# Optimization experiments

Measured on AMD Instinct MI355X. Metric: run time of the kernel, lower is better.

The kernel has to match this reference:

```python
import jax, jax.numpy as jnp
import numpy as np

HEADS = 8
SR = 4
EPS = 1e-5


def _ln(x, g, b):
    m = jnp.mean(x, -1, keepdims=True)
    v = jnp.mean(jnp.square(x - m), -1, keepdims=True)
    return (x - m) / jnp.sqrt(v + EPS) * g + b


def _conv3d(x, w, b, stride, pad, groups=1):
    # x: [B,C,H,W,Z]; w: [O, I/groups, kH, kW, kZ]
    y = jax.lax.conv_general_dilated(x, w, window_strides=stride, padding=pad,
                                     dimension_numbers=('NCHWD', 'OIHWD', 'NCHWD'),
                                     feature_group_count=groups)
    return y + b[None, :, None, None, None]


def setup_inputs() -> dict:
    key = jax.random.key(0)
    B, H, W, Z, C = 1, 32, 32, 8, 256
    N = H * W * Z
    ks = jax.random.split(key, 10)
    s = 0.02
    return {
        'x': jax.random.normal(ks[0], (B, N, C), jnp.float32),
        'Wq': jax.random.normal(ks[1], (C, C), jnp.float32) * s,
        'sr1_w': jax.random.normal(ks[2], (C, C, 4, 4, 1), jnp.float32) * 0.03,
        'sr1_b': jnp.zeros((C,), jnp.float32),
        'ln1_w': jnp.ones((C,), jnp.float32),
        'ln1_b': jnp.zeros((C,), jnp.float32),
        'sr2_w': jax.random.normal(ks[3], (C, C, 2, 2, 1), jnp.float32) * 0.06,
        'sr2_b': jnp.zeros((C,), jnp.float32),
        'ln2_w': jnp.ones((C,), jnp.float32),
        'ln2_b': jnp.zeros((C,), jnp.float32),
        'Wkv1': jax.random.normal(ks[4], (C, C), jnp.float32) * s,
        'Wkv2': jax.random.normal(ks[5], (C, C), jnp.float32) * s,
        'lc1_w': jax.random.normal(ks[6], (C // 2, 1, 3, 3, 1), jnp.float32) * 0.3,
        'lc1_b': jnp.zeros((C // 2,), jnp.float32),
        'lc2_w': jax.random.normal(ks[7], (C // 2, 1, 3, 3, 1), jnp.float32) * 0.3,
        'lc2_b': jnp.zeros((C // 2,), jnp.float32),
        'proj_w': jax.random.normal(ks[8], (C, C), jnp.float32) * s,
        'proj_b': jnp.zeros((C,), jnp.float32),
        'H': H, 'W': W, 'Z': Z,
    }


def reference(x, Wq, sr1_w, sr1_b, ln1_w, ln1_b, sr2_w, sr2_b, ln2_w, ln2_b,
              Wkv1, Wkv2, lc1_w, lc1_b, lc2_w, lc2_b, proj_w, proj_b, H, W, Z):
    B, N, C = x.shape
    hd = C // HEADS
    h2 = HEADS // 2
    scale = hd ** -0.5
    # q: [B, heads, N, hd]
    q = (x @ Wq.T).reshape(B, N, HEADS, hd).transpose(0, 2, 1, 3)
    x_ = x.transpose(0, 2, 1).reshape(B, C, H, W, Z)

    def branch(sr_w, sr_b, stride, ln_w, ln_b, Wkv, lc_w, lc_b, q_h, Hs, Ws):
        # spatial-reduction conv -> LN -> GELU (exact erf, as torch nn.GELU)
        xr = _conv3d(x_, sr_w, sr_b, stride, 'VALID').reshape(B, C, -1).transpose(0, 2, 1)
        xr = jax.nn.gelu(_ln(xr, ln_w, ln_b), approximate=False)  # [B, M, C]
        kv = (xr @ Wkv.T).reshape(B, -1, 2, h2, hd).transpose(2, 0, 3, 1, 4)
        k, v = kv[0], kv[1]  # [B, h2, M, hd]
        a = jax.nn.softmax(jnp.einsum('bhnd,bhmd->bhnm', q_h, k) * scale, axis=-1)
        # depthwise 3x3x1 conv added into V
        vg = v.transpose(0, 2, 1, 3).reshape(B, -1, C // 2).transpose(0, 2, 1)
        vg = vg.reshape(B, C // 2, Hs, Ws, Z)
        vg = _conv3d(vg, lc_w, lc_b, (1, 1, 1), ((1, 1), (1, 1), (0, 0)), groups=C // 2)
        v = v + vg.reshape(B, h2, hd, -1).transpose(0, 1, 3, 2)
        return jnp.einsum('bhnm,bhmd->bhnd', a, v).transpose(0, 2, 1, 3).reshape(B, N, C // 2)

    x1 = branch(sr1_w, sr1_b, (SR, SR, 1), ln1_w, ln1_b, Wkv1, lc1_w, lc1_b,
                q[:, :h2], H // SR, W // SR)
    x2 = branch(sr2_w, sr2_b, (SR // 2, SR // 2, 1), ln2_w, ln2_b, Wkv2, lc2_w, lc2_b,
                q[:, h2:], H * 2 // SR, W * 2 // SR)
    return jnp.concatenate([x1, x2], axis=-1) @ proj_w.T + proj_b
```

## Files before the change

### kernel.cpp

```cpp
#include <hip/hip_runtime.h>
#include <math.h>

#define C_DIM 256
#define HH 32
#define WW 32
#define ZZ 8
#define HD 32

typedef __attribute__((ext_vector_type(8))) short bf16x8;
typedef __attribute__((ext_vector_type(4))) float f32x4;
typedef __attribute__((ext_vector_type(4))) unsigned int u32x4;

__device__ inline unsigned short f2bf(float f) {
    unsigned int u = __builtin_bit_cast(unsigned int, f);
    u += 0x7FFF + ((u >> 16) & 1);
    return (unsigned short)(u >> 16);
}
__device__ inline unsigned int cvtpk_bf16(float a, float b) {
    unsigned int r;
    asm("v_cvt_pk_bf16_f32 %0, %1, %2" : "=v"(r) : "v"(a), "v"(b));
    return r;
}

#define QSCALE (0.17677669529663689f * 1.4426950408889634f)

template <bool ABF16>
__global__ __launch_bounds__(256) void gemm_split_kernel(
    const void* __restrict__ Av, const float* __restrict__ B,
    const float* __restrict__ bias, float* __restrict__ C,
    int M, int N, int K,
    unsigned short* __restrict__ qb_out) {
    __shared__ unsigned short Ah[2][2560], Al[2][2560], Bh[2][2560], Bl[2][2560];
    int t = threadIdx.x;
    int wave = t >> 6, lane = t & 63;
    int lg = lane >> 4, lc = lane & 15;
    int wm = wave >> 1, wn = wave & 1;
    int m0 = blockIdx.y * 64, n0 = blockIdx.x * 64;
    int Kc = K / gridDim.z;
    int kbeg = blockIdx.z * Kc;
    float* Cz = C + (long)blockIdx.z * M * N;
    int srow = t >> 2, sc8 = (t & 3) * 8;
    const float* aBaseF = ABF16 ? nullptr : (const float*)Av + (long)(m0 + srow) * K + kbeg + sc8;
    const unsigned short* aBaseH = ABF16 ? (const unsigned short*)Av + (long)(m0 + srow) * K + kbeg + sc8 : nullptr;
    const float* bBase = B + (long)(n0 + srow) * K + kbeg + sc8;
    int nIter = Kc / 32;

    f32x4 acc[2][2];
#pragma unroll
    for (int i = 0; i < 2; ++i)
#pragma unroll
        for (int j = 0; j < 2; ++j) acc[i][j] = (f32x4){0.f, 0.f, 0.f, 0.f};

    auto split8 = [](f32x4 v0, f32x4 v1, u32x4& hw, u32x4& lw) {
        float av[8] = {v0[0], v0[1], v0[2], v0[3], v1[0], v1[1], v1[2], v1[3]};
#pragma unroll
        for (int p = 0; p < 4; ++p) {
            float x0 = av[2 * p], x1 = av[2 * p + 1];
            unsigned int w = cvtpk_bf16(x0, x1);
            float h0 = __builtin_bit_cast(float, w << 16);
            float h1 = __builtin_bit_cast(float, w & 0xFFFF0000u);
            hw[p] = w;
            lw[p] = cvtpk_bf16(x0 - h0, x1 - h1);
        }
    };

    auto stage = [&](int buf, int k) {
        if constexpr (ABF16) {
            u32x4 aw = *reinterpret_cast<const u32x4*>(aBaseH + k * 32);
            *reinterpret_cast<u32x4*>(&Ah[buf][srow * 40 + sc8]) = aw;
        } else {
            f32x4 a0 = *reinterpret_cast<const f32x4*>(aBaseF + k * 32);
            f32x4 a1 = *reinterpret_cast<const f32x4*>(aBaseF + k * 32 + 4);
            u32x4 hw, lw;
            split8(a0, a1, hw, lw);
            *reinterpret_cast<u32x4*>(&Ah[buf][srow * 40 + sc8]) = hw;
            *reinterpret_cast<u32x4*>(&Al[buf][srow * 40 + sc8]) = lw;
        }
        f32x4 b0 = *reinterpret_cast<const f32x4*>(bBase + k * 32);
        f32x4 b1 = *reinterpret_cast<const f32x4*>(bBase + k * 32 + 4);
        u32x4 hw, lw;
        split8(b0, b1, hw, lw);
        *reinterpret_cast<u32x4*>(&Bh[buf][srow * 40 + sc8]) = hw;
        *reinterpret_cast<u32x4*>(&Bl[buf][srow * 40 + sc8]) = lw;
    };

    stage(0, 0);
    __syncthreads();

    for (int k = 0; k < nIter; ++k) {
        int cur = k & 1;
        bool more = (k + 1 < nIter);
        bf16x8 afh[2], afl[2], bfh[2], bfl[2];
#pragma unroll
        for (int i = 0; i < 2; ++i) {
            int ar = wm * 32 + i * 16 + lc;
            afh[i] = *reinterpret_cast<const bf16x8*>(&Ah[cur][ar * 40 + lg * 8]);
            if constexpr (!ABF16)
                afl[i] = *reinterpret_cast<const bf16x8*>(&Al[cur][ar * 40 + lg * 8]);
            int br = wn * 32 + i * 16 + lc;
            bfh[i] = *reinterpret_cast<const bf16x8*>(&Bh[cur][br * 40 + lg * 8]);
            bfl[i] = *reinterpret_cast<const bf16x8*>(&Bl[cur][br * 40 + lg * 8]);
        }
#pragma unroll
        for (int i = 0; i < 2; ++i)
#pragma unroll
            for (int j = 0; j < 2; ++j) {
                acc[i][j] = __builtin_amdgcn_mfma_f32_16x16x32_bf16(afh[i], bfh[j], acc[i][j], 0, 0, 0);
                acc[i][j] = __builtin_amdgcn_mfma_f32_16x16x32_bf16(afh[i], bfl[j], acc[i][j], 0, 0, 0);
                if constexpr (!ABF16)
                    acc[i][j] = __builtin_amdgcn_mfma_f32_16x16x32_bf16(afl[i], bfh[j], acc[i][j], 0, 0, 0);
            }
        if (more) {
            stage(cur ^ 1, k + 1);
            __syncthreads();
        }
    }
#pragma unroll
    for (int i = 0; i < 2; ++i)
#pragma unroll
        for (int j = 0; j < 2; ++j)
#pragma unroll
            for (int r = 0; r < 4; ++r) {
                int row = m0 + wm * 32 + i * 16 + lg * 4 + r;
                int col = n0 + wn * 32 + j * 16 + lc;
                float bv = bias ? bias[col] : 0.f;
                float val = acc[i][j][r] + bv;
                if (qb_out) {
                    qb_out[(long)row * N + col] = f2bf(val * QSCALE);
                } else {
                    Cz[(long)row * N + col] = val;
                }
            }
}

__global__ void reduce_ln_gelu_fused_kernel(
    const float* __restrict__ p1, const float* __restrict__ b1f,
    const float* __restrict__ g1, const float* __restrict__ bb1, float* __restrict__ x1,
    const float* __restrict__ p2, const float* __restrict__ b2f,
    const float* __restrict__ g2, const float* __restrict__ bb2, float* __restrict__ x2) {
    int bx = blockIdx.x;
    int br1 = (bx < 512);
    int m = br1 ? bx : bx - 512;
    const float* part = br1 ? p1 : p2;
    const float* bias = br1 ? b1f : b2f;
    const float* g = br1 ? g1 : g2;
    const float* bb = br1 ? bb1 : bb2;
    float* xr = br1 ? x1 : x2;
    int MN = br1 ? 512 * 256 : 2048 * 256;
    int KS = br1 ? 16 : 4;

    int c = threadIdx.x;
    float v = bias[c];
    for (int z = 0; z < KS; ++z) v += part[(long)z * MN + m * C_DIM + c];
    __shared__ float wred[4];
    float s = v;
    for (int off = 32; off; off >>= 1) s += __shfl_down(s, off);
    if ((c & 63) == 0) wred[c >> 6] = s;
    __syncthreads();
    float mean = (wred[0] + wred[1] + wred[2] + wred[3]) * (1.f / 256.f);
    __syncthreads();
    float d = v - mean;
    float s2 = d * d;
    for (int off = 32; off; off >>= 1) s2 += __shfl_down(s2, off);
    if ((c & 63) == 0) wred[c >> 6] = s2;
    __syncthreads();
    float var = (wred[0] + wred[1] + wred[2] + wred[3]) * (1.f / 256.f);
    float y = d * rsqrtf(var + 1e-5f) * g[c] + bb[c];
    float ge = 0.5f * y * (1.f + erff(y * 0.70710678118654752f));
    xr[m * C_DIM + c] = ge;
}

__global__ void reduce_kv_fused_kernel(
    const float* __restrict__ p1, float* __restrict__ kv1, unsigned short* __restrict__ kb1,
    const float* __restrict__ p2, float* __restrict__ kv2, unsigned short* __restrict__ kb2) {
    int bx = blockIdx.x;
    int br1 = (bx < 512);
    int m = br1 ? bx : bx - 512;
    const float* part = br1 ? p1 : p2;
    float* kv = br1 ? kv1 : kv2;
    unsigned short* kb = br1 ? kb1 : kb2;
    int MN = br1 ? 512 * 256 : 2048 * 256;
    int KS = br1 ? 8 : 4;
    int KTp = br1 ? 4 : 16;

    int c = threadIdx.x;
    float v = 0.f;
    for (int z = 0; z < KS; ++z) v += part[(long)z * MN + m * C_DIM + c];
    kv[m * C_DIM + c] = v;
    if (c < 128) {
        int h = c >> 5, cc = c & 31, kt = m >> 7, mi = m & 127;
        kb[((long)(h * KTp + kt) * 128 + mi) * 32 + cc] = f2bf(v);
    }
}

template <int S>
__global__ void im2col_kernel(const float* __restrict__ x, float* __restrict__ im, int Ws) {
    constexpr int T = S * S;
    __shared__ float patch[T * 257];
    int m = blockIdx.x;
    int z = m % ZZ;
    int wo = (m / ZZ) % Ws;
    int ho = m / (ZZ * Ws);
    int t = threadIdx.x;
#pragma unroll
    for (int tap = 0; tap < T; ++tap) {
        int kh = tap / S, kw = tap % S;
        int row = (ho * S + kh) * (WW * ZZ) + (wo * S + kw) * ZZ + z;
        patch[tap * 257 + t] = x[row * C_DIM + t];
    }
    __syncthreads();
#pragma unroll
    for (int rep = 0; rep < T; ++rep) {
        int k = rep * 256 + t;
        int ci = k / T, tap = k % T;
        im[(long)m * (256 * T) + k] = patch[tap * 257 + ci];
    }
}

__global__ void dw_conv_fused_kernel(const float* __restrict__ kv1, const float* __restrict__ lw1,
                                     const float* __restrict__ lb1, unsigned short* __restrict__ vt1,
                                     const float* __restrict__ kv2, const float* __restrict__ lw2,
                                     const float* __restrict__ lb2, unsigned short* __restrict__ vt2) {
    int bx = blockIdx.x;
    int b1 = (bx < 512);
    int m = b1 ? bx : bx - 512;
    const float* kv = b1 ? kv1 : kv2;
    const float* lw = b1 ? lw1 : lw2;
    const float* lb = b1 ? lb1 : lb2;
    unsigned short* vt = b1 ? vt1 : vt2;
    int Ws = b1 ? 8 : 16, Hs = b1 ? 8 : 16, KT = b1 ? 4 : 16;

    int ch = threadIdx.x;
    int z = m % ZZ;
    int wo = (m / ZZ) % Ws;
    int ho = m / (ZZ * Ws);
    float acc = lb[ch];
#pragma unroll
    for (int kh = 0; kh < 3; ++kh) {
        int h = ho + kh - 1;
        if (h < 0 || h >= Hs) continue;
#pragma unroll
        for (int kw = 0; kw < 3; ++kw) {
            int w2 = wo + kw - 1;
            if (w2 < 0 || w2 >= Ws) continue;
            int mm = (h * Ws + w2) * ZZ + z;
            acc += kv[mm * C_DIM + 128 + ch] * lw[ch * 9 + kh * 3 + kw];
        }
    }
    int hh = ch >> 5, d = ch & 31, kt = m >> 7, mi = m & 127;
    int a = mi >> 5, u = (mi >> 4) & 1, g = (mi >> 2) & 3, v = mi & 3;
    int s = (a << 5) | (g << 3) | (u << 2) | v;
    vt[((long)(hh * KT + kt) * 32 + d) * 128 + s] = f2bf(kv[m * C_DIM + 128 + ch] + acc);
}

__global__ __launch_bounds__(256, 2) void attn_fused_kernel(
    const unsigned short* __restrict__ qb,
    const unsigned short* __restrict__ kb1, const unsigned short* __restrict__ vt1,
    const unsigned short* __restrict__ kb2, const unsigned short* __restrict__ vt2,
    unsigned short* __restrict__ catb) {
    int wave = threadIdx.x >> 6;
    int lane = threadIdx.x & 63;
    int lg = lane >> 4;
    int lc = lane & 15;
    int by = blockIdx.y;
    int big = ((by >> 2) == 0);
    int head = by & 3;
    const unsigned short* kb = big ? kb2 : kb1;
    const unsigned short* vt = big ? vt2 : vt1;
    int KT = big ? 16 : 4;
    int col_base = big ? 128 : 0;
    int q0 = blockIdx.x * 128 + wave * 32;

    bf16x8 qf0 = *reinterpret_cast<const bf16x8*>(qb + (long)(q0 + lc) * C_DIM + col_base + head * HD + lg * 8);
    bf16x8 qf1 = *reinterpret_cast<const bf16x8*>(qb + (long)(q0 + 16 + lc) * C_DIM + col_base + head * HD + lg * 8);

    const unsigned short* kbase = kb + (long)head * KT * 4096;
    const unsigned short* vbase = vt + (long)head * KT * 4096;

    f32x4 o00 = {0.f, 0.f, 0.f, 0.f}, o01 = {0.f, 0.f, 0.f, 0.f};
    f32x4 o10 = {0.f, 0.f, 0.f, 0.f}, o11 = {0.f, 0.f, 0.f, 0.f};
    float lsum0 = 0.f, lsum1 = 0.f;

    bf16x8 kf[8];
    bf16x8 vf0c[4], vf1c[4];
#pragma unroll
    for (int c = 0; c < 8; ++c)
        kf[c] = *reinterpret_cast<const bf16x8*>(kbase + (16 * c + lc) * 32 + lg * 8);
#pragma unroll
    for (int c2 = 0; c2 < 4; ++c2) {
        vf0c[c2] = *reinterpret_cast<const bf16x8*>(vbase + lc * 128 + c2 * 32 + lg * 8);
        vf1c[c2] = *reinterpret_cast<const bf16x8*>(vbase + (16 + lc) * 128 + c2 * 32 + lg * 8);
    }

    for (int kt = 0; kt < KT; ++kt) {
        f32x4 s0[8], s1[8];
        f32x4 z = {0.f, 0.f, 0.f, 0.f};
#pragma unroll
        for (int c = 0; c < 8; ++c) {
            s0[c] = __builtin_amdgcn_mfma_f32_16x16x32_bf16(kf[c], qf0, z, 0, 0, 0);
            s1[c] = __builtin_amdgcn_mfma_f32_16x16x32_bf16(kf[c], qf1, z, 0, 0, 0);
        }
        bf16x8 vf0n[4], vf1n[4];
        if (kt + 1 < KT) {
            const unsigned short* knext = kbase + (long)(kt + 1) * 4096;
            const unsigned short* vnext = vbase + (long)(kt + 1) * 4096;
#pragma unroll
            for (int c = 0; c < 8; ++c)
                kf[c] = *reinterpret_cast<const bf16x8*>(knext + (16 * c + lc) * 32 + lg * 8);
#pragma unroll
            for (int c2 = 0; c2 < 4; ++c2) {
                vf0n[c2] = *reinterpret_cast<const bf16x8*>(vnext + lc * 128 + c2 * 32 + lg * 8);
                vf1n[c2] = *reinterpret_cast<const bf16x8*>(vnext + (16 + lc) * 128 + c2 * 32 + lg * 8);
            }
        }
#pragma unroll
        for (int c2 = 0; c2 < 4; ++c2) {
            unsigned int w0, w1, w2, w3;
            {
                int c = 2 * c2;
                float p0 = __builtin_amdgcn_exp2f(s0[c][0]);
                float p1 = __builtin_amdgcn_exp2f(s0[c][1]);
                float p2 = __builtin_amdgcn_exp2f(s0[c][2]);
                float p3 = __builtin_amdgcn_exp2f(s0[c][3]);
                lsum0 += (p0 + p1) + (p2 + p3);
                w0 = cvtpk_bf16(p0, p1);
                w1 = cvtpk_bf16(p2, p3);
            }
            {
                int c = 2 * c2 + 1;
                float p0 = __builtin_amdgcn_exp2f(s0[c][0]);
                float p1 = __builtin_amdgcn_exp2f(s0[c][1]);
                float p2 = __builtin_amdgcn_exp2f(s0[c][2]);
                float p3 = __builtin_amdgcn_exp2f(s0[c][3]);
                lsum0 += (p0 + p1) + (p2 + p3);
                w2 = cvtpk_bf16(p0, p1);
                w3 = cvtpk_bf16(p2, p3);
            }
            u32x4 pw = {w0, w1, w2, w3};
            bf16x8 pa = __builtin_bit_cast(bf16x8, pw);
            o00 = __builtin_amdgcn_mfma_f32_16x16x32_bf16(pa, vf0c[c2], o00, 0, 0, 0);
            o01 = __builtin_amdgcn_mfma_f32_16x16x32_bf16(pa, vf1c[c2], o01, 0, 0, 0);
        }
#pragma unroll
        for (int c2 = 0; c2 < 4; ++c2) {
            unsigned int w0, w1, w2, w3;
            {
                int c = 2 * c2;
                float p0 = __builtin_amdgcn_exp2f(s1[c][0]);
                float p1 = __builtin_amdgcn_exp2f(s1[c][1]);
                float p2 = __builtin_amdgcn_exp2f(s1[c][2]);
                float p3 = __builtin_amdgcn_exp2f(s1[c][3]);
                lsum1 += (p0 + p1) + (p2 + p3);
                w0 = cvtpk_bf16(p0, p1);
                w1 = cvtpk_bf16(p2, p3);
            }
            {
                int c = 2 * c2 + 1;
                float p0 = __builtin_amdgcn_exp2f(s1[c][0]);
                float p1 = __builtin_amdgcn_exp2f(s1[c][1]);
                float p2 = __builtin_amdgcn_exp2f(s1[c][2]);
                float p3 = __builtin_amdgcn_exp2f(s1[c][3]);
                lsum1 += (p0 + p1) + (p2 + p3);
                w2 = cvtpk_bf16(p0, p1);
                w3 = cvtpk_bf16(p2, p3);
            }
            u32x4 pw = {w0, w1, w2, w3};
            bf16x8 pa = __builtin_bit_cast(bf16x8, pw);
            o10 = __builtin_amdgcn_mfma_f32_16x16x32_bf16(pa, vf0c[c2], o10, 0, 0, 0);
            o11 = __builtin_amdgcn_mfma_f32_16x16x32_bf16(pa, vf1c[c2], o11, 0, 0, 0);
        }
        if (kt + 1 < KT) {
#pragma unroll
            for (int c2 = 0; c2 < 4; ++c2) {
                vf0c[c2] = vf0n[c2];
                vf1c[c2] = vf1n[c2];
            }
        }
    }
    lsum0 += __shfl_xor(lsum0, 16);
    lsum0 += __shfl_xor(lsum0, 32);
    lsum1 += __shfl_xor(lsum1, 16);
    lsum1 += __shfl_xor(lsum1, 32);
#pragma unroll
    for (int r = 0; r < 4; ++r) {
        float ls = __shfl(lsum0, lg * 4 + r);
        float inv = 1.f / ls;
        int row = q0 + lg * 4 + r;
        catb[(long)row * C_DIM + col_base + head * HD + lc] = f2bf(o00[r] * inv);
        catb[(long)row * C_DIM + col_base + head * HD + 16 + lc] = f2bf(o01[r] * inv);
    }
#pragma unroll
    for (int r = 0; r < 4; ++r) {
        float ls = __shfl(lsum1, lg * 4 + r);
        float inv = 1.f / ls;
        int row = q0 + 16 + lg * 4 + r;
        catb[(long)row * C_DIM + col_base + head * HD + lc] = f2bf(o10[r] * inv);
        catb[(long)row * C_DIM + col_base + head * HD + 16 + lc] = f2bf(o11[r] * inv);
    }
}

extern "C" void kernel_launch(void* const* d_in, const int* in_sizes, int n_in,
                              void* d_out, int out_size, void* d_ws, size_t ws_size,
                              hipStream_t stream) {
    const float* x      = (const float*)d_in[0];
    const float* Wq     = (const float*)d_in[1];
    const float* sr1_w  = (const float*)d_in[2];
    const float* sr1_b  = (const float*)d_in[3];
    const float* ln1_w  = (const float*)d_in[4];
    const float* ln1_b  = (const float*)d_in[5];
    const float* sr2_w  = (const float*)d_in[6];
    const float* sr2_b  = (const float*)d_in[7];
    const float* ln2_w  = (const float*)d_in[8];
    const float* ln2_b  = (const float*)d_in[9];
    const float* Wkv1   = (const float*)d_in[10];
    const float* Wkv2   = (const float*)d_in[11];
    const float* lc1_w  = (const float*)d_in[12];
    const float* lc1_b  = (const float*)d_in[13];
    const float* lc2_w  = (const float*)d_in[14];
    const float* lc2_b  = (const float*)d_in[15];
    const float* proj_w = (const float*)d_in[16];
    const float* proj_b = (const float*)d_in[17];
    float* out = (float*)d_out;
    char* wsb = (char*)d_ws;

    float* buf0 = (float*)wsb;
    unsigned short* qb = (unsigned short*)(wsb + 8388608);
    float* im = (float*)(wsb + 12582912);
    float* xr1 = (float*)(wsb + 20971520);
    float* kv1 = (float*)(wsb + 21495808);
    unsigned short* kb1 = (unsigned short*)(wsb + 22020096);
    unsigned short* vt1 = (unsigned short*)(wsb + 22151168);
    float* xr2 = (float*)(wsb + 22282240);
    float* kv2 = (float*)(wsb + 24379392);
    unsigned short* kb2 = (unsigned short*)(wsb + 26476544);
    unsigned short* vt2 = (unsigned short*)(wsb + 27000832);
    float* hi = (float*)(wsb + 27525120);

    float* part1 = buf0;
    float* part2 = hi;
    float* kv1part = buf0;
    float* kv2part = im;
    unsigned short* catb = (unsigned short*)hi;

    gemm_split_kernel<false><<<dim3(4, 128, 1), 256, 0, stream>>>(x, Wq, nullptr, (float*)qb, 8192, 256, 256, qb);

    im2col_kernel<4><<<512, 256, 0, stream>>>(x, im, 8);
    gemm_split_kernel<false><<<dim3(4, 8, 16), 256, 0, stream>>>(im, sr1_w, nullptr, part1, 512, 256, 4096, nullptr);
    im2col_kernel<2><<<2048, 256, 0, stream>>>(x, im, 16);
    gemm_split_kernel<false><<<dim3(4, 32, 4), 256, 0, stream>>>(im, sr2_w, nullptr, part2, 2048, 256, 1024, nullptr);

    reduce_ln_gelu_fused_kernel<<<2560, 256, 0, stream>>>(part1, sr1_b, ln1_w, ln1_b, xr1,
                                                          part2, sr2_b, ln2_w, ln2_b, xr2);

    gemm_split_kernel<false><<<dim3(4, 8, 8), 256, 0, stream>>>(xr1, Wkv1, nullptr, kv1part, 512, 256, 256, nullptr);
    gemm_split_kernel<false><<<dim3(4, 32, 4), 256, 0, stream>>>(xr2, Wkv2, nullptr, kv2part, 2048, 256, 256, nullptr);

    reduce_kv_fused_kernel<<<2560, 256, 0, stream>>>(kv1part, kv1, kb1, kv2part, kv2, kb2);

    dw_conv_fused_kernel<<<2560, 128, 0, stream>>>(kv1, lc1_w, lc1_b, vt1, kv2, lc2_w, lc2_b, vt2);

    attn_fused_kernel<<<dim3(64, 8), 256, 0, stream>>>(qb, kb1, vt1, kb2, vt2, catb);

    gemm_split_kernel<true><<<dim3(4, 128, 1), 256, 0, stream>>>(catb, proj_w, proj_b, out, 8192, 256, 256, nullptr);
}
```

Before: 119.0 us.

## Merge Q and SR-conv GEMMs into one launch, batch KV GEMMs together

Result: faster. 99.76 us (-16.1%).

```diff
diff --git a/kernel.cpp b/kernel.cpp
--- a/kernel.cpp
+++ b/kernel.cpp
@@ -24,24 +24,23 @@
 
 #define QSCALE (0.17677669529663689f * 1.4426950408889634f)
 
-template <bool ABF16>
-__global__ __launch_bounds__(256) void gemm_split_kernel(
-    const void* __restrict__ Av, const float* __restrict__ B,
+__device__ __forceinline__ void gemm_job(
+    const float* __restrict__ A, const float* __restrict__ B,
     const float* __restrict__ bias, float* __restrict__ C,
-    int M, int N, int K,
-    unsigned short* __restrict__ qb_out) {
-    __shared__ unsigned short Ah[2][2560], Al[2][2560], Bh[2][2560], Bl[2][2560];
+    int M, int N, int K, int KS, int z, int bx, int by,
+    unsigned short* __restrict__ qb_out,
+    unsigned short (*Ah)[2560], unsigned short (*Al)[2560],
+    unsigned short (*Bh)[2560], unsigned short (*Bl)[2560]) {
     int t = threadIdx.x;
     int wave = t >> 6, lane = t & 63;
     int lg = lane >> 4, lc = lane & 15;
     int wm = wave >> 1, wn = wave & 1;
-    int m0 = blockIdx.y * 64, n0 = blockIdx.x * 64;
-    int Kc = K / gridDim.z;
-    int kbeg = blockIdx.z * Kc;
-    float* Cz = C + (long)blockIdx.z * M * N;
+    int m0 = by * 64, n0 = bx * 64;
+    int Kc = K / KS;
+    int kbeg = z * Kc;
+    float* Cz = C + (long)z * M * N;
     int srow = t >> 2, sc8 = (t & 3) * 8;
-    const float* aBaseF = ABF16 ? nullptr : (const float*)Av + (long)(m0 + srow) * K + kbeg + sc8;
-    const unsigned short* aBaseH = ABF16 ? (const unsigned short*)Av + (long)(m0 + srow) * K + kbeg + sc8 : nullptr;
+    const float* aBase = A + (long)(m0 + srow) * K + kbeg + sc8;
     const float* bBase = B + (long)(n0 + srow) * K + kbeg + sc8;
     int nIter = Kc / 32;
 
@@ -63,22 +62,15 @@
             lw[p] = cvtpk_bf16(x0 - h0, x1 - h1);
         }
     };
-
     auto stage = [&](int buf, int k) {
-        if constexpr (ABF16) {
-            u32x4 aw = *reinterpret_cast<const u32x4*>(aBaseH + k * 32);
-            *reinterpret_cast<u32x4*>(&Ah[buf][srow * 40 + sc8]) = aw;
-        } else {
-            f32x4 a0 = *reinterpret_cast<const f32x4*>(aBaseF + k * 32);
-            f32x4 a1 = *reinterpret_cast<const f32x4*>(aBaseF + k * 32 + 4);
-            u32x4 hw, lw;
-            split8(a0, a1, hw, lw);
-            *reinterpret_cast<u32x4*>(&Ah[buf][srow * 40 + sc8]) = hw;
-            *reinterpret_cast<u32x4*>(&Al[buf][srow * 40 + sc8]) = lw;
-        }
+        f32x4 a0 = *reinterpret_cast<const f32x4*>(aBase + k * 32);
+        f32x4 a1 = *reinterpret_cast<const f32x4*>(aBase + k * 32 + 4);
+        u32x4 hw, lw;
+        split8(a0, a1, hw, lw);
+        *reinterpret_cast<u32x4*>(&Ah[buf][srow * 40 + sc8]) = hw;
+        *reinterpret_cast<u32x4*>(&Al[buf][srow * 40 + sc8]) = lw;
         f32x4 b0 = *reinterpret_cast<const f32x4*>(bBase + k * 32);
         f32x4 b1 = *reinterpret_cast<const f32x4*>(bBase + k * 32 + 4);
-        u32x4 hw, lw;
         split8(b0, b1, hw, lw);
         *reinterpret_cast<u32x4*>(&Bh[buf][srow * 40 + sc8]) = hw;
         *reinterpret_cast<u32x4*>(&Bl[buf][srow * 40 + sc8]) = lw;
@@ -95,8 +87,7 @@
         for (int i = 0; i < 2; ++i) {
             int ar = wm * 32 + i * 16 + lc;
             afh[i] = *reinterpret_cast<const bf16x8*>(&Ah[cur][ar * 40 + lg * 8]);
-            if constexpr (!ABF16)
-                afl[i] = *reinterpret_cast<const bf16x8*>(&Al[cur][ar * 40 + lg * 8]);
+            afl[i] = *reinterpret_cast<const bf16x8*>(&Al[cur][ar * 40 + lg * 8]);
             int br = wn * 32 + i * 16 + lc;
             bfh[i] = *reinterpret_cast<const bf16x8*>(&Bh[cur][br * 40 + lg * 8]);
             bfl[i] = *reinterpret_cast<const bf16x8*>(&Bl[cur][br * 40 + lg * 8]);
@@ -107,8 +98,7 @@
             for (int j = 0; j < 2; ++j) {
                 acc[i][j] = __builtin_amdgcn_mfma_f32_16x16x32_bf16(afh[i], bfh[j], acc[i][j], 0, 0, 0);
                 acc[i][j] = __builtin_amdgcn_mfma_f32_16x16x32_bf16(afh[i], bfl[j], acc[i][j], 0, 0, 0);
-                if constexpr (!ABF16)
-                    acc[i][j] = __builtin_amdgcn_mfma_f32_16x16x32_bf16(afl[i], bfh[j], acc[i][j], 0, 0, 0);
+                acc[i][j] = __builtin_amdgcn_mfma_f32_16x16x32_bf16(afl[i], bfh[j], acc[i][j], 0, 0, 0);
             }
         if (more) {
             stage(cur ^ 1, k + 1);
@@ -130,6 +120,119 @@
                 } else {
                     Cz[(long)row * N + col] = val;
                 }
+            }
+}
+
+__global__ __launch_bounds__(256) void qsr_fused_kernel(
+    const float* __restrict__ x, const float* __restrict__ Wq,
+    unsigned short* __restrict__ qb,
+    const float* __restrict__ im1, const float* __restrict__ sr1_w, float* __restrict__ part1,
+    const float* __restrict__ im2, const float* __restrict__ sr2_w, float* __restrict__ part2) {
+    __shared__ unsigned short Ah[2][2560], Al[2][2560], Bh[2][2560], Bl[2][2560];
+    int b = blockIdx.x;
+    if (b < 512) {
+        gemm_job(x, Wq, nullptr, nullptr, 8192, 256, 256, 1, 0, b & 3, b >> 2, qb, Ah, Al, Bh, Bl);
+    } else if (b < 768) {
+        int l = b - 512;
+        gemm_job(im1, sr1_w, nullptr, part1, 512, 256, 4096, 8, l >> 5, l & 3, (l >> 2) & 7, nullptr, Ah, Al, Bh, Bl);
+    } else {
+        int l = b - 768;
+        gemm_job(im2, sr2_w, nullptr, part2, 2048, 256, 1024, 2, l >> 7, l & 3, (l >> 2) & 31, nullptr, Ah, Al, Bh, Bl);
+    }
+}
+
+__global__ __launch_bounds__(256) void kv_fused_gemm_kernel(
+    const float* __restrict__ xr1, const float* __restrict__ Wkv1, float* __restrict__ kv1part,
+    const float* __restrict__ xr2, const float* __restrict__ Wkv2, float* __restrict__ kv2part) {
+    __shared__ unsigned short Ah[2][2560], Al[2][2560], Bh[2][2560], Bl[2][2560];
+    int b = blockIdx.x;
+    if (b < 256) {
+        gemm_job(xr1, Wkv1, nullptr, kv1part, 512, 256, 256, 8, b >> 5, b & 3, (b >> 2) & 7, nullptr, Ah, Al, Bh, Bl);
+    } else {
+        int l = b - 256;
+        gemm_job(xr2, Wkv2, nullptr, kv2part, 2048, 256, 256, 4, l >> 7, l & 3, (l >> 2) & 31, nullptr, Ah, Al, Bh, Bl);
+    }
+}
+
+__global__ __launch_bounds__(256) void gemm_projb_kernel(
+    const unsigned short* __restrict__ A, const float* __restrict__ B,
+    const float* __restrict__ bias, float* __restrict__ C, int M, int N, int K) {
+    __shared__ unsigned short Ah[2][2560], Bh[2][2560], Bl[2][2560];
+    int t = threadIdx.x;
+    int wave = t >> 6, lane = t & 63;
+    int lg = lane >> 4, lc = lane & 15;
+    int wm = wave >> 1, wn = wave & 1;
+    int m0 = blockIdx.y * 64, n0 = blockIdx.x * 64;
+    int srow = t >> 2, sc8 = (t & 3) * 8;
+    const unsigned short* aBase = A + (long)(m0 + srow) * K + sc8;
+    const float* bBase = B + (long)(n0 + srow) * K + sc8;
+    int nIter = K / 32;
+
+    f32x4 acc[2][2];
+#pragma unroll
+    for (int i = 0; i < 2; ++i)
+#pragma unroll
+        for (int j = 0; j < 2; ++j) acc[i][j] = (f32x4){0.f, 0.f, 0.f, 0.f};
+
+    auto split8 = [](f32x4 v0, f32x4 v1, u32x4& hw, u32x4& lw) {
+        float av[8] = {v0[0], v0[1], v0[2], v0[3], v1[0], v1[1], v1[2], v1[3]};
+#pragma unroll
+        for (int p = 0; p < 4; ++p) {
+            float x0 = av[2 * p], x1 = av[2 * p + 1];
+            unsigned int w = cvtpk_bf16(x0, x1);
+            float h0 = __builtin_bit_cast(float, w << 16);
+            float h1 = __builtin_bit_cast(float, w & 0xFFFF0000u);
+            hw[p] = w;
+            lw[p] = cvtpk_bf16(x0 - h0, x1 - h1);
+        }
+    };
+    auto stage = [&](int buf, int k) {
+        u32x4 aw = *reinterpret_cast<const u32x4*>(aBase + k * 32);
+        *reinterpret_cast<u32x4*>(&Ah[buf][srow * 40 + sc8]) = aw;
+        f32x4 b0 = *reinterpret_cast<const f32x4*>(bBase + k * 32);
+        f32x4 b1 = *reinterpret_cast<const f32x4*>(bBase + k * 32 + 4);
+        u32x4 hw, lw;
+        split8(b0, b1, hw, lw);
+        *reinterpret_cast<u32x4*>(&Bh[buf][srow * 40 + sc8]) = hw;
+        *reinterpret_cast<u32x4*>(&Bl[buf][srow * 40 + sc8]) = lw;
+    };
+
+    stage(0, 0);
+    __syncthreads();
+
+    for (int k = 0; k < nIter; ++k) {
+        int cur = k & 1;
+        bool more = (k + 1 < nIter);
+        bf16x8 af[2], bfh[2], bfl[2];
+#pragma unroll
+        for (int i = 0; i < 2; ++i) {
+            int ar = wm * 32 + i * 16 + lc;
+            af[i] = *reinterpret_cast<const bf16x8*>(&Ah[cur][ar * 40 + lg * 8]);
+            int br = wn * 32 + i * 16 + lc;
+            bfh[i] = *reinterpret_cast<const bf16x8*>(&Bh[cur][br * 40 + lg * 8]);
+            bfl[i] = *reinterpret_cast<const bf16x8*>(&Bl[cur][br * 40 + lg * 8]);
+        }
+#pragma unroll
+        for (int i = 0; i < 2; ++i)
+#pragma unroll
+            for (int j = 0; j < 2; ++j) {
+                acc[i][j] = __builtin_amdgcn_mfma_f32_16x16x32_bf16(af[i], bfh[j], acc[i][j], 0, 0, 0);
+                acc[i][j] = __builtin_amdgcn_mfma_f32_16x16x32_bf16(af[i], bfl[j], acc[i][j], 0, 0, 0);
+            }
+        if (more) {
+            stage(cur ^ 1, k + 1);
+            __syncthreads();
+        }
+    }
+#pragma unroll
+    for (int i = 0; i < 2; ++i)
+#pragma unroll
+        for (int j = 0; j < 2; ++j)
+#pragma unroll
+            for (int r = 0; r < 4; ++r) {
+                int row = m0 + wm * 32 + i * 16 + lg * 4 + r;
+                int col = n0 + wn * 32 + j * 16 + lc;
+                C[(long)row * N + col] = acc[i][j][r] + bias[col];
             }
 }
 
@@ -147,7 +250,7 @@
     const float* bb = br1 ? bb1 : bb2;
     float* xr = br1 ? x1 : x2;
     int MN = br1 ? 512 * 256 : 2048 * 256;
-    int KS = br1 ? 16 : 4;
+    int KS = br1 ? 8 : 2;
 
     int c = threadIdx.x;
     float v = bias[c];
@@ -436,24 +539,23 @@
     unsigned short* vt2 = (unsigned short*)(wsb + 27000832);
     float* hi = (float*)(wsb + 27525120);
 
+    float* im1 = hi;
+    float* im2 = im;
     float* part1 = buf0;
-    float* part2 = hi;
+    float* part2 = (float*)(wsb + 4194304);
     float* kv1part = buf0;
     float* kv2part = im;
     unsigned short* catb = (unsigned short*)hi;
 
-    gemm_split_kernel<false><<<dim3(4, 128, 1), 256, 0, stream>>>(x, Wq, nullptr, (float*)qb, 8192, 256, 256, qb);
-
-    im2col_kernel<4><<<512, 256, 0, stream>>>(x, im, 8);
-    gemm_split_kernel<false><<<dim3(4, 8, 16), 256, 0, stream>>>(im, sr1_w, nullptr, part1, 512, 256, 4096, nullptr);
-    im2col_kernel<2><<<2048, 256, 0, stream>>>(x, im, 16);
-    gemm_split_kernel<false><<<dim3(4, 32, 4), 256, 0, stream>>>(im, sr2_w, nullptr, part2, 2048, 256, 1024, nullptr);
+    im2col_kernel<4><<<512, 256, 0, stream>>>(x, im1, 8);
+    im2col_kernel<2><<<2048, 256, 0, stream>>>(x, im2, 16);
+
+    qsr_fused_kernel<<<1024, 256, 0, stream>>>(x, Wq, qb, im1, sr1_w, part1, im2, sr2_w, part2);
 
     reduce_ln_gelu_fused_kernel<<<2560, 256, 0, stream>>>(part1, sr1_b, ln1_w, ln1_b, xr1,
                                                           part2, sr2_b, ln2_w, ln2_b, xr2);
 
-    gemm_split_kernel<false><<<dim3(4, 8, 8), 256, 0, stream>>>(xr1, Wkv1, nullptr, kv1part, 512, 256, 256, nullptr);
-    gemm_split_kernel<false><<<dim3(4, 32, 4), 256, 0, stream>>>(xr2, Wkv2, nullptr, kv2part, 2048, 256, 256, nullptr);
+    kv_fused_gemm_kernel<<<768, 256, 0, stream>>>(xr1, Wkv1, kv1part, xr2, Wkv2, kv2part);
 
     reduce_kv_fused_kernel<<<2560, 256, 0, stream>>>(kv1part, kv1, kb1, kv2part, kv2, kb2);
 
@@ -461,5 +563,5 @@
 
     attn_fused_kernel<<<dim3(64, 8), 256, 0, stream>>>(qb, kb1, vt1, kb2, vt2, catb);
 
-    gemm_split_kernel<true><<<dim3(4, 128, 1), 256, 0, stream>>>(catb, proj_w, proj_b, out, 8192, 256, 256, nullptr);
-}
+    gemm_projb_kernel<<<dim3(4, 128), 256, 0, stream>>>(catb, proj_w, proj_b, out, 8192, 256, 256);
+}
```
